# Kernel optimization log

Measured on AMD Instinct MI355X. Metric: run time of the kernel, lower is better.

The kernel has to match this reference:

```python
import jax, jax.numpy as jnp
import numpy as np

L, S, N, E, H = 2048, 2048, 4, 1024, 16
D = E // H  # head_dim = 64


def setup_inputs() -> dict:
    key = jax.random.key(0)
    ks = jax.random.split(key, 7)
    scale = 1.0 / np.sqrt(E)
    return {
        "query": jax.random.normal(ks[0], (L, N, E), jnp.float32),
        "key": jax.random.normal(ks[1], (S, N, E), jnp.float32),
        "value": jax.random.normal(ks[2], (S, N, E), jnp.float32),
        "in_proj_w": jax.random.normal(ks[3], (3 * E, E), jnp.float32) * scale,
        "in_proj_b": jax.random.normal(ks[4], (3 * E,), jnp.float32) * 0.01,
        "out_proj_w": jax.random.normal(ks[5], (E, E), jnp.float32) * scale * 0.25,
        "out_proj_b": jax.random.normal(ks[6], (E,), jnp.float32) * 0.01,
    }


def reference(query, key, value, in_proj_w, in_proj_b, out_proj_w, out_proj_b):
    # Split packed in-projection into q/k/v parts (torch layout: [3E, E]).
    wq, wk, wv = in_proj_w[:E], in_proj_w[E:2 * E], in_proj_w[2 * E:]
    bq, bk, bv = in_proj_b[:E], in_proj_b[E:2 * E], in_proj_b[2 * E:]

    def proj(x, w, b):  # (T,N,E) -> (N,H,T,D)
        y = jnp.einsum('tne,fe->tnf', x, w) + b
        T = x.shape[0]
        return y.reshape(T, N, H, D).transpose(1, 2, 0, 3)

    q = proj(query, wq, bq) * (1.0 / np.sqrt(D))  # scale queries
    k = proj(key, wk, bk)
    v = proj(value, wv, bv)

    scores = jnp.einsum('nhld,nhsd->nhls', q, k)  # (N,H,L,S)
    attn = jax.nn.softmax(scores, axis=-1)
    ctx = jnp.einsum('nhls,nhsd->nhld', attn, v)  # (N,H,L,D)
    ctx = ctx.transpose(2, 0, 1, 3).reshape(L, N, E)  # (L,N,E)

    out = jnp.einsum('lne,fe->lnf', ctx, out_proj_w) + out_proj_b
    attn_weights = attn.mean(axis=1)  # (N,L,S), averaged over heads (torch default)
    return out, attn_weights
```

## Files before the change

kernel.cpp:

```cpp
#include <hip/hip_runtime.h>
#include <hip/hip_bf16.h>

#define L_ 2048
#define S_ 2048
#define NB 4
#define E_ 1024
#define H_ 16
#define D_ 64
#define LDT 72

typedef __attribute__((ext_vector_type(8))) short bf16x8;
typedef __attribute__((ext_vector_type(4))) float f32x4;

__device__ __forceinline__ short f2bf(float f) {
  union { float f; unsigned u; } v; v.f = f;
  unsigned r = v.u + 0x7FFFu + ((v.u >> 16) & 1u);
  return (short)(r >> 16);
}
__device__ __forceinline__ float bf2f(short s) {
  union { unsigned u; float f; } v; v.u = ((unsigned)(unsigned short)s) << 16;
  return v.f;
}

__global__ void k_convert(const float* __restrict__ wi, const float* __restrict__ wo,
                          short* __restrict__ wqkv, short* __restrict__ wout) {
  const int n1 = 3 * E_ * E_ / 4;
  const int n2 = E_ * E_ / 4;
  const int stride = gridDim.x * blockDim.x;
  for (int i = blockIdx.x * blockDim.x + threadIdx.x; i < n1 + n2; i += stride) {
    const float4* s; short* d; int j;
    if (i < n1) { s = (const float4*)wi; d = wqkv; j = i; }
    else        { s = (const float4*)wo; d = wout; j = i - n1; }
    float4 v = s[j];
    short4 o = make_short4(f2bf(v.x), f2bf(v.y), f2bf(v.z), f2bf(v.w));
    *(short4*)&d[(size_t)j * 4] = o;
  }
}

__global__ __launch_bounds__(256) void k_qkv(
    const float* __restrict__ qin, const float* __restrict__ kin, const float* __restrict__ vin,
    const short* __restrict__ wbf, const float* __restrict__ bias,
    short* __restrict__ qh, short* __restrict__ kh, short* __restrict__ vh) {
  __shared__ short As[128 * LDT];
  __shared__ short Bs[128 * LDT];
  const int bm = blockIdx.x;
  const int fbase = blockIdx.y * 128;
  const int mat = fbase >> 10;
  const float* __restrict__ A = (mat == 0) ? qin : (mat == 1) ? kin : vin;
  short* __restrict__ dst = (mat == 0) ? qh : (mat == 1) ? kh : vh;
  const float scale = (mat == 0) ? 0.125f : 1.0f;
  const int tid = threadIdx.x;
  const int lane = tid & 63, wid = tid >> 6;
  const int wr = wid >> 1, wc = wid & 1;
  const int lr = lane & 15, lk = lane >> 4;
  f32x4 acc[4][4] = {};

  for (int kb = 0; kb < E_; kb += 64) {
#pragma unroll
    for (int i = 0; i < 8; ++i) {
      int f4 = i * 256 + tid;
      int row = f4 >> 4, k4 = f4 & 15;
      float4 v = *(const float4*)&A[(size_t)(bm * 128 + row) * E_ + kb + k4 * 4];
      short4 o = make_short4(f2bf(v.x), f2bf(v.y), f2bf(v.z), f2bf(v.w));
      *(short4*)&As[row * LDT + k4 * 4] = o;
    }
#pragma unroll
    for (int i = 0; i < 4; ++i) {
      int e8 = i * 256 + tid;
      int row = e8 >> 3, k8 = e8 & 7;
      int4 v = *(const int4*)&wbf[(size_t)(fbase + row) * E_ + kb + k8 * 8];
      *(int4*)&Bs[row * LDT + k8 * 8] = v;
    }
    __syncthreads();
#pragma unroll
    for (int kk = 0; kk < 2; ++kk) {
      bf16x8 a[4], b[4];
#pragma unroll
      for (int fi = 0; fi < 4; ++fi)
        a[fi] = *(const bf16x8*)&As[(wr * 64 + fi * 16 + lr) * LDT + kk * 32 + lk * 8];
#pragma unroll
      for (int ci = 0; ci < 4; ++ci)
        b[ci] = *(const bf16x8*)&Bs[(wc * 64 + ci * 16 + lr) * LDT + kk * 32 + lk * 8];
#pragma unroll
      for (int fi = 0; fi < 4; ++fi)
#pragma unroll
        for (int ci = 0; ci < 4; ++ci)
          acc[fi][ci] = __builtin_amdgcn_mfma_f32_16x16x32_bf16(a[fi], b[ci], acc[fi][ci], 0, 0, 0);
    }
    __syncthreads();
  }
#pragma unroll
  for (int ci = 0; ci < 4; ++ci) {
    const int fg = fbase + wc * 64 + ci * 16 + lr;
    const float b = bias[fg];
    const int col = fg & 1023;
    const int h = col >> 6, d = col & 63;
#pragma unroll
    for (int fi = 0; fi < 4; ++fi)
#pragma unroll
      for (int j = 0; j < 4; ++j) {
        int m = bm * 128 + wr * 64 + fi * 16 + lk * 4 + j;
        int t = m >> 2, n = m & 3;
        float vv = (acc[fi][ci][j] + b) * scale;
        dst[(((size_t)(n * H_ + h) * L_ + t) << 6) + d] = f2bf(vv);
      }
  }
}

__global__ __launch_bounds__(256) void k_stats(
    const short* __restrict__ qh, const short* __restrict__ kh, float* __restrict__ rl) {
  const int nh = blockIdx.y;
  const int qt = blockIdx.x;
  const short* __restrict__ Q = qh + (size_t)nh * L_ * D_;
  const short* __restrict__ K = kh + (size_t)nh * S_ * D_;
  const int tid = threadIdx.x;
  const int lane = tid & 63, wid = tid >> 6;
  const int lr = lane & 15, lk = lane >> 4;
  const int rbase = qt * 128 + wid * 32;
  bf16x8 a[2][2];
#pragma unroll
  for (int ri = 0; ri < 2; ++ri)
#pragma unroll
    for (int kk = 0; kk < 2; ++kk)
      a[ri][kk] = *(const bf16x8*)&Q[(size_t)(rbase + ri * 16 + lr) * D_ + kk * 32 + lk * 8];
  float ssum[2][4] = {};
  for (int st = 0; st < S_; st += 64) {
    f32x4 acc[2][4] = {};
#pragma unroll
    for (int ci = 0; ci < 4; ++ci) {
      bf16x8 b0 = *(const bf16x8*)&K[(size_t)(st + ci * 16 + lr) * D_ + lk * 8];
      bf16x8 b1 = *(const bf16x8*)&K[(size_t)(st + ci * 16 + lr) * D_ + 32 + lk * 8];
#pragma unroll
      for (int ri = 0; ri < 2; ++ri) {
        acc[ri][ci] = __builtin_amdgcn_mfma_f32_16x16x32_bf16(a[ri][0], b0, acc[ri][ci], 0, 0, 0);
        acc[ri][ci] = __builtin_amdgcn_mfma_f32_16x16x32_bf16(a[ri][1], b1, acc[ri][ci], 0, 0, 0);
      }
    }
#pragma unroll
    for (int ri = 0; ri < 2; ++ri)
#pragma unroll
      for (int j = 0; j < 4; ++j) {
        float s = __expf(acc[ri][0][j]) + __expf(acc[ri][1][j]) +
                  __expf(acc[ri][2][j]) + __expf(acc[ri][3][j]);
        s += __shfl_xor(s, 1);
        s += __shfl_xor(s, 2);
        s += __shfl_xor(s, 4);
        s += __shfl_xor(s, 8);
        ssum[ri][j] += s;
      }
  }
  if (lr == 0) {
#pragma unroll
    for (int ri = 0; ri < 2; ++ri)
#pragma unroll
      for (int j = 0; j < 4; ++j)
        rl[(size_t)nh * L_ + rbase + ri * 16 + lk * 4 + j] = 1.0f / ssum[ri][j];
  }
}

__global__ __launch_bounds__(1024) void k_attn(
    const short* __restrict__ qh, const short* __restrict__ kh, const short* __restrict__ vh,
    const float* __restrict__ rl, float* __restrict__ attnw, short* __restrict__ ctx) {
  __shared__ short psl[16][32 * 40];
  const int n = blockIdx.y, qt = blockIdx.x;
  const int tid = threadIdx.x;
  const int h = tid >> 6, lane = tid & 63;
  const int lr = lane & 15, lk = lane >> 4;
  const size_t nh = (size_t)(n * H_ + h);
  const short* __restrict__ Q = qh + nh * L_ * D_;
  const short* __restrict__ K = kh + nh * S_ * D_;
  const short* __restrict__ V = vh + nh * S_ * D_;
  const int rbase = qt * 32;
  bf16x8 a[2][2];
#pragma unroll
  for (int ri = 0; ri < 2; ++ri)
#pragma unroll
    for (int kk = 0; kk < 2; ++kk)
      a[ri][kk] = *(const bf16x8*)&Q[(size_t)(rbase + ri * 16 + lr) * D_ + kk * 32 + lk * 8];
  float rls[2][4];
#pragma unroll
  for (int ri = 0; ri < 2; ++ri)
#pragma unroll
    for (int j = 0; j < 4; ++j)
      rls[ri][j] = rl[nh * L_ + rbase + ri * 16 + lk * 4 + j];
  f32x4 cacc[2][4] = {};

  for (int st = 0; st < S_; st += 32) {
    f32x4 sacc[2][2] = {};
#pragma unroll
    for (int ci = 0; ci < 2; ++ci) {
      bf16x8 b0 = *(const bf16x8*)&K[(size_t)(st + ci * 16 + lr) * D_ + lk * 8];
      bf16x8 b1 = *(const bf16x8*)&K[(size_t)(st + ci * 16 + lr) * D_ + 32 + lk * 8];
#pragma unroll
      for (int ri = 0; ri < 2; ++ri) {
        sacc[ri][ci] = __builtin_amdgcn_mfma_f32_16x16x32_bf16(a[ri][0], b0, sacc[ri][ci], 0, 0, 0);
        sacc[ri][ci] = __builtin_amdgcn_mfma_f32_16x16x32_bf16(a[ri][1], b1, sacc[ri][ci], 0, 0, 0);
      }
    }
#pragma unroll
    for (int ri = 0; ri < 2; ++ri)
#pragma unroll
      for (int ci = 0; ci < 2; ++ci)
#pragma unroll
        for (int j = 0; j < 4; ++j) {
          float p = __expf(sacc[ri][ci][j]) * rls[ri][j];
          psl[h][(ri * 16 + lk * 4 + j) * 40 + ci * 16 + lr] = f2bf(p);
        }
    bf16x8 pa[2];
#pragma unroll
    for (int ri = 0; ri < 2; ++ri)
      pa[ri] = *(const bf16x8*)&psl[h][(ri * 16 + lr) * 40 + lk * 8];
#pragma unroll
    for (int ci = 0; ci < 4; ++ci) {
      bf16x8 vb;
#pragma unroll
      for (int e = 0; e < 8; ++e)
        vb[e] = V[(size_t)(st + lk * 8 + e) * D_ + ci * 16 + lr];
#pragma unroll
      for (int ri = 0; ri < 2; ++ri)
        cacc[ri][ci] = __builtin_amdgcn_mfma_f32_16x16x32_bf16(pa[ri], vb, cacc[ri][ci], 0, 0, 0);
    }
    __syncthreads();
    {
      const int ml = tid >> 5, ms = tid & 31;
      float s = 0.f;
#pragma unroll
      for (int w = 0; w < 16; ++w) s += bf2f(psl[w][ml * 40 + ms]);
      attnw[((size_t)n * L_ + rbase + ml) * S_ + st + ms] = s * 0.0625f;
    }
    __syncthreads();
  }
#pragma unroll
  for (int ri = 0; ri < 2; ++ri)
#pragma unroll
    for (int ci = 0; ci < 4; ++ci)
#pragma unroll
      for (int j = 0; j < 4; ++j) {
        int row = rbase + ri * 16 + lk * 4 + j;
        int d = ci * 16 + lr;
        ctx[((size_t)row * NB + n) * E_ + h * 64 + d] = f2bf(cacc[ri][ci][j]);
      }
}

__global__ __launch_bounds__(256) void k_out(
    const short* __restrict__ ctxb, const short* __restrict__ wbf,
    const float* __restrict__ bias, float* __restrict__ out) {
  __shared__ short As[128 * LDT];
  __shared__ short Bs[128 * LDT];
  const int bm = blockIdx.x, bn = blockIdx.y;
  const int tid = threadIdx.x;
  const int lane = tid & 63, wid = tid >> 6;
  const int wr = wid >> 1, wc = wid & 1;
  const int lr = lane & 15, lk = lane >> 4;
  f32x4 acc[4][4] = {};
  for (int kb = 0; kb < E_; kb += 64) {
#pragma unroll
    for (int i = 0; i < 4; ++i) {
      int e8 = i * 256 + tid;
      int row = e8 >> 3, k8 = e8 & 7;
      int4 va = *(const int4*)&ctxb[(size_t)(bm * 128 + row) * E_ + kb + k8 * 8];
      *(int4*)&As[row * LDT + k8 * 8] = va;
      int4 vb = *(const int4*)&wbf[(size_t)(bn * 128 + row) * E_ + kb + k8 * 8];
      *(int4*)&Bs[row * LDT + k8 * 8] = vb;
    }
    __syncthreads();
#pragma unroll
    for (int kk = 0; kk < 2; ++kk) {
      bf16x8 a[4], b[4];
#pragma unroll
      for (int fi = 0; fi < 4; ++fi)
        a[fi] = *(const bf16x8*)&As[(wr * 64 + fi * 16 + lr) * LDT + kk * 32 + lk * 8];
#pragma unroll
      for (int ci = 0; ci < 4; ++ci)
        b[ci] = *(const bf16x8*)&Bs[(wc * 64 + ci * 16 + lr) * LDT + kk * 32 + lk * 8];
#pragma unroll
      for (int fi = 0; fi < 4; ++fi)
#pragma unroll
        for (int ci = 0; ci < 4; ++ci)
          acc[fi][ci] = __builtin_amdgcn_mfma_f32_16x16x32_bf16(a[fi], b[ci], acc[fi][ci], 0, 0, 0);
    }
    __syncthreads();
  }
#pragma unroll
  for (int ci = 0; ci < 4; ++ci) {
    int col = bn * 128 + wc * 64 + ci * 16 + lr;
    float b = bias[col];
#pragma unroll
    for (int fi = 0; fi < 4; ++fi)
#pragma unroll
      for (int j = 0; j < 4; ++j) {
        int m = bm * 128 + wr * 64 + fi * 16 + lk * 4 + j;
        out[(size_t)m * E_ + col] = acc[fi][ci][j] + b;
      }
  }
}

extern "C" void kernel_launch(void* const* d_in, const int* in_sizes, int n_in,
                              void* d_out, int out_size, void* d_ws, size_t ws_size,
                              hipStream_t stream) {
  const float* qin = (const float*)d_in[0];
  const float* kin = (const float*)d_in[1];
  const float* vin = (const float*)d_in[2];
  const float* wi  = (const float*)d_in[3];
  const float* bi  = (const float*)d_in[4];
  const float* wo  = (const float*)d_in[5];
  const float* bo  = (const float*)d_in[6];
  float* out = (float*)d_out;
  float* attnw = out + (size_t)L_ * NB * E_;

  short* wqkv = (short*)d_ws;
  short* wout = wqkv + (size_t)3 * E_ * E_;
  short* qh = wout + (size_t)E_ * E_;
  short* kh = qh + (size_t)NB * L_ * E_;
  short* vh = kh + (size_t)NB * L_ * E_;
  float* rl = (float*)(vh + (size_t)NB * L_ * E_);
  short* ctx = (short*)(rl + (size_t)NB * H_ * L_);

  k_convert<<<1024, 256, 0, stream>>>(wi, wo, wqkv, wout);
  k_qkv<<<dim3(64, 24), 256, 0, stream>>>(qin, kin, vin, wqkv, bi, qh, kh, vh);
  k_stats<<<dim3(16, 64), 256, 0, stream>>>(qh, kh, rl);
  k_attn<<<dim3(64, 4), 1024, 0, stream>>>(qh, kh, vh, rl, attnw, ctx);
  k_out<<<dim3(64, 8), 256, 0, stream>>>(ctx, wout, bo, out);
}
```

Baseline: 555.5 us.

## Pre-transpose V, fold log2e into Q, swap QK operand order for vectorized stores

Adds a kernel that transposes V per head so the attention kernel loads V fragments as contiguous 8-element vectors instead of eight strided scalar loads. Folds log2(e) into the Q scaling so softmax uses the native exp2 instruction in both the stats and attention kernels. Swaps the MFMA operand order to compute S^T, so probabilities are written to LDS as packed short4, and the head-averaging pass now reads pairs of bf16 and writes float2 using half the threads. It costs an extra kernel launch plus workspace for the transposed V copy.

Result: faster. 511.5 us (-7.9%).

```diff
diff --git a/kernel.cpp b/kernel.cpp
--- a/kernel.cpp
+++ b/kernel.cpp
@@ -16,10 +16,6 @@
   union { float f; unsigned u; } v; v.f = f;
   unsigned r = v.u + 0x7FFFu + ((v.u >> 16) & 1u);
   return (short)(r >> 16);
-}
-__device__ __forceinline__ float bf2f(short s) {
-  union { unsigned u; float f; } v; v.u = ((unsigned)(unsigned short)s) << 16;
-  return v.f;
 }
 
 __global__ void k_convert(const float* __restrict__ wi, const float* __restrict__ wo,
@@ -48,7 +44,7 @@
   const int mat = fbase >> 10;
   const float* __restrict__ A = (mat == 0) ? qin : (mat == 1) ? kin : vin;
   short* __restrict__ dst = (mat == 0) ? qh : (mat == 1) ? kh : vh;
-  const float scale = (mat == 0) ? 0.125f : 1.0f;
+  const float scale = (mat == 0) ? 0.125f * 1.44269504088896f : 1.0f;
   const int tid = threadIdx.x;
   const int lane = tid & 63, wid = tid >> 6;
   const int wr = wid >> 1, wc = wid & 1;
@@ -107,6 +103,32 @@
   }
 }
 
+__global__ __launch_bounds__(256) void k_vtrans(const short* __restrict__ vh,
+                                                short* __restrict__ vt) {
+  __shared__ short t[64][LDT];
+  const int nh = blockIdx.y;
+  const int tb = blockIdx.x;
+  const int tid = threadIdx.x;
+  const short* __restrict__ src = vh + ((size_t)nh * L_ + tb * 64) * D_;
+  short* __restrict__ dst = vt + (size_t)nh * D_ * S_ + tb * 64;
+#pragma unroll
+  for (int i = 0; i < 2; ++i) {
+    int v = i * 256 + tid;
+    int r = v >> 3, c8 = v & 7;
+    *(bf16x8*)&t[r][c8 * 8] = *(const bf16x8*)&src[(size_t)r * D_ + c8 * 8];
+  }
+  __syncthreads();
+#pragma unroll
+  for (int i = 0; i < 2; ++i) {
+    int v = i * 256 + tid;
+    int d = v >> 3, t8 = v & 7;
+    bf16x8 o;
+#pragma unroll
+    for (int e = 0; e < 8; ++e) o[e] = t[t8 * 8 + e][d];
+    *(bf16x8*)&dst[(size_t)d * S_ + t8 * 8] = o;
+  }
+}
+
 __global__ __launch_bounds__(256) void k_stats(
     const short* __restrict__ qh, const short* __restrict__ kh, float* __restrict__ rl) {
   const int nh = blockIdx.y;
@@ -140,8 +162,8 @@
     for (int ri = 0; ri < 2; ++ri)
 #pragma unroll
       for (int j = 0; j < 4; ++j) {
-        float s = __expf(acc[ri][0][j]) + __expf(acc[ri][1][j]) +
-                  __expf(acc[ri][2][j]) + __expf(acc[ri][3][j]);
+        float s = __builtin_amdgcn_exp2f(acc[ri][0][j]) + __builtin_amdgcn_exp2f(acc[ri][1][j]) +
+                  __builtin_amdgcn_exp2f(acc[ri][2][j]) + __builtin_amdgcn_exp2f(acc[ri][3][j]);
         s += __shfl_xor(s, 1);
         s += __shfl_xor(s, 2);
         s += __shfl_xor(s, 4);
@@ -159,7 +181,7 @@
 }
 
 __global__ __launch_bounds__(1024) void k_attn(
-    const short* __restrict__ qh, const short* __restrict__ kh, const short* __restrict__ vh,
+    const short* __restrict__ qh, const short* __restrict__ kh, const short* __restrict__ vt,
     const float* __restrict__ rl, float* __restrict__ attnw, short* __restrict__ ctx) {
   __shared__ short psl[16][32 * 40];
   const int n = blockIdx.y, qt = blockIdx.x;
@@ -169,76 +191,82 @@
   const size_t nh = (size_t)(n * H_ + h);
   const short* __restrict__ Q = qh + nh * L_ * D_;
   const short* __restrict__ K = kh + nh * S_ * D_;
-  const short* __restrict__ V = vh + nh * S_ * D_;
+  const short* __restrict__ VT = vt + nh * D_ * S_;
   const int rbase = qt * 32;
-  bf16x8 a[2][2];
-#pragma unroll
-  for (int ri = 0; ri < 2; ++ri)
+  bf16x8 qf[2][2];
+#pragma unroll
+  for (int li = 0; li < 2; ++li)
 #pragma unroll
     for (int kk = 0; kk < 2; ++kk)
-      a[ri][kk] = *(const bf16x8*)&Q[(size_t)(rbase + ri * 16 + lr) * D_ + kk * 32 + lk * 8];
-  float rls[2][4];
-#pragma unroll
-  for (int ri = 0; ri < 2; ++ri)
-#pragma unroll
-    for (int j = 0; j < 4; ++j)
-      rls[ri][j] = rl[nh * L_ + rbase + ri * 16 + lk * 4 + j];
+      qf[li][kk] = *(const bf16x8*)&Q[(size_t)(rbase + li * 16 + lr) * D_ + kk * 32 + lk * 8];
+  float rls[2];
+#pragma unroll
+  for (int li = 0; li < 2; ++li)
+    rls[li] = rl[nh * L_ + rbase + li * 16 + lr];
   f32x4 cacc[2][4] = {};
+  const int mrow = tid >> 4, mcp = tid & 15;
+  float* awp = attnw + ((size_t)n * L_ + rbase + mrow) * S_;
 
   for (int st = 0; st < S_; st += 32) {
     f32x4 sacc[2][2] = {};
 #pragma unroll
-    for (int ci = 0; ci < 2; ++ci) {
-      bf16x8 b0 = *(const bf16x8*)&K[(size_t)(st + ci * 16 + lr) * D_ + lk * 8];
-      bf16x8 b1 = *(const bf16x8*)&K[(size_t)(st + ci * 16 + lr) * D_ + 32 + lk * 8];
-#pragma unroll
-      for (int ri = 0; ri < 2; ++ri) {
-        sacc[ri][ci] = __builtin_amdgcn_mfma_f32_16x16x32_bf16(a[ri][0], b0, sacc[ri][ci], 0, 0, 0);
-        sacc[ri][ci] = __builtin_amdgcn_mfma_f32_16x16x32_bf16(a[ri][1], b1, sacc[ri][ci], 0, 0, 0);
-      }
-    }
-#pragma unroll
-    for (int ri = 0; ri < 2; ++ri)
-#pragma unroll
-      for (int ci = 0; ci < 2; ++ci)
-#pragma unroll
-        for (int j = 0; j < 4; ++j) {
-          float p = __expf(sacc[ri][ci][j]) * rls[ri][j];
-          psl[h][(ri * 16 + lk * 4 + j) * 40 + ci * 16 + lr] = f2bf(p);
-        }
+    for (int si = 0; si < 2; ++si) {
+      bf16x8 k0 = *(const bf16x8*)&K[(size_t)(st + si * 16 + lr) * D_ + lk * 8];
+      bf16x8 k1 = *(const bf16x8*)&K[(size_t)(st + si * 16 + lr) * D_ + 32 + lk * 8];
+#pragma unroll
+      for (int li = 0; li < 2; ++li) {
+        sacc[si][li] = __builtin_amdgcn_mfma_f32_16x16x32_bf16(k0, qf[li][0], sacc[si][li], 0, 0, 0);
+        sacc[si][li] = __builtin_amdgcn_mfma_f32_16x16x32_bf16(k1, qf[li][1], sacc[si][li], 0, 0, 0);
+      }
+    }
+    bf16x8 vb[4];
+#pragma unroll
+    for (int ci = 0; ci < 4; ++ci)
+      vb[ci] = *(const bf16x8*)&VT[(size_t)(ci * 16 + lr) * S_ + st + lk * 8];
+#pragma unroll
+    for (int si = 0; si < 2; ++si)
+#pragma unroll
+      for (int li = 0; li < 2; ++li) {
+        short4 pk;
+        pk.x = f2bf(__builtin_amdgcn_exp2f(sacc[si][li][0]) * rls[li]);
+        pk.y = f2bf(__builtin_amdgcn_exp2f(sacc[si][li][1]) * rls[li]);
+        pk.z = f2bf(__builtin_amdgcn_exp2f(sacc[si][li][2]) * rls[li]);
+        pk.w = f2bf(__builtin_amdgcn_exp2f(sacc[si][li][3]) * rls[li]);
+        *(short4*)&psl[h][(li * 16 + lr) * 40 + si * 16 + lk * 4] = pk;
+      }
     bf16x8 pa[2];
 #pragma unroll
-    for (int ri = 0; ri < 2; ++ri)
-      pa[ri] = *(const bf16x8*)&psl[h][(ri * 16 + lr) * 40 + lk * 8];
-#pragma unroll
-    for (int ci = 0; ci < 4; ++ci) {
-      bf16x8 vb;
-#pragma unroll
-      for (int e = 0; e < 8; ++e)
-        vb[e] = V[(size_t)(st + lk * 8 + e) * D_ + ci * 16 + lr];
-#pragma unroll
-      for (int ri = 0; ri < 2; ++ri)
-        cacc[ri][ci] = __builtin_amdgcn_mfma_f32_16x16x32_bf16(pa[ri], vb, cacc[ri][ci], 0, 0, 0);
-    }
-    __syncthreads();
-    {
-      const int ml = tid >> 5, ms = tid & 31;
-      float s = 0.f;
-#pragma unroll
-      for (int w = 0; w < 16; ++w) s += bf2f(psl[w][ml * 40 + ms]);
-      attnw[((size_t)n * L_ + rbase + ml) * S_ + st + ms] = s * 0.0625f;
-    }
-    __syncthreads();
-  }
-#pragma unroll
-  for (int ri = 0; ri < 2; ++ri)
+    for (int li = 0; li < 2; ++li)
+      pa[li] = *(const bf16x8*)&psl[h][(li * 16 + lr) * 40 + lk * 8];
 #pragma unroll
     for (int ci = 0; ci < 4; ++ci)
 #pragma unroll
+      for (int li = 0; li < 2; ++li)
+        cacc[li][ci] = __builtin_amdgcn_mfma_f32_16x16x32_bf16(pa[li], vb[ci], cacc[li][ci], 0, 0, 0);
+    __syncthreads();
+    if (tid < 512) {
+      float s0 = 0.f, s1 = 0.f;
+#pragma unroll
+      for (int w = 0; w < 16; ++w) {
+        unsigned u = *(const unsigned*)&psl[w][mrow * 40 + mcp * 2];
+        union { unsigned u; float f; } a, b;
+        a.u = u << 16; b.u = u & 0xFFFF0000u;
+        s0 += a.f; s1 += b.f;
+      }
+      float2 o = make_float2(s0 * 0.0625f, s1 * 0.0625f);
+      *(float2*)&awp[st + mcp * 2] = o;
+    }
+    __syncthreads();
+  }
+#pragma unroll
+  for (int li = 0; li < 2; ++li)
+#pragma unroll
+    for (int ci = 0; ci < 4; ++ci)
+#pragma unroll
       for (int j = 0; j < 4; ++j) {
-        int row = rbase + ri * 16 + lk * 4 + j;
+        int row = rbase + li * 16 + lk * 4 + j;
         int d = ci * 16 + lr;
-        ctx[((size_t)row * NB + n) * E_ + h * 64 + d] = f2bf(cacc[ri][ci][j]);
+        ctx[((size_t)row * NB + n) * E_ + h * 64 + d] = f2bf(cacc[li][ci][j]);
       }
 }
 
@@ -313,12 +341,14 @@
   short* qh = wout + (size_t)E_ * E_;
   short* kh = qh + (size_t)NB * L_ * E_;
   short* vh = kh + (size_t)NB * L_ * E_;
-  float* rl = (float*)(vh + (size_t)NB * L_ * E_);
+  short* vt = vh + (size_t)NB * L_ * E_;
+  float* rl = (float*)(vt + (size_t)NB * L_ * E_);
   short* ctx = (short*)(rl + (size_t)NB * H_ * L_);
 
   k_convert<<<1024, 256, 0, stream>>>(wi, wo, wqkv, wout);
   k_qkv<<<dim3(64, 24), 256, 0, stream>>>(qin, kin, vin, wqkv, bi, qh, kh, vh);
+  k_vtrans<<<dim3(32, 64), 256, 0, stream>>>(vh, vt);
   k_stats<<<dim3(16, 64), 256, 0, stream>>>(qh, kh, rl);
-  k_attn<<<dim3(64, 4), 1024, 0, stream>>>(qh, kh, vh, rl, attnw, ctx);
+  k_attn<<<dim3(64, 4), 1024, 0, stream>>>(qh, kh, vt, rl, attnw, ctx);
   k_out<<<dim3(64, 8), 256, 0, stream>>>(ctx, wout, bo, out);
 }
```
